# Kernel optimization log

Measured on AMD Instinct MI355X. Metric: run time of the kernel, lower is better.

## Reference

```python
import jax, jax.numpy as jnp
import numpy as np

LOG2PI = 1.8378770664093453
KL_WEIGHT = 1.0
N_OBS = 2_000_000
N_REFL = 250_000
N_IMG = 2000
MC = 32
N_OPS = 2
D_META = 6
D_EMB = 32
D_IN = 2 + 2 + D_META + 2 + D_EMB  # Imodel(2) + Iscale(2) + metadata(6) + wavelength + 1/d^2 + image embed
HIDDEN = 64


def weighted_pearson(x, y, w):
    z = 1.0 / w.sum(-1)
    mx = z * (w * x).sum(-1)
    my = z * (w * y).sum(-1)
    dx = x - mx
    dy = y - my
    cxy = z * (w * dx * dy).sum(-1)
    cx = z * (w * dx * dx).sum(-1)
    cy = z * (w * dy * dy).sum(-1)
    return cxy / jnp.sqrt(cx * cy)


def setup_inputs() -> dict:
    key = jax.random.key(0)
    ks = jax.random.split(key, 16)
    I = jax.random.normal(ks[0], (N_OBS, 1), jnp.float32)
    SigI = jax.random.uniform(ks[1], (N_OBS, 1), jnp.float32, 0.5, 1.5)
    image_id = jnp.sort(jax.random.randint(ks[2], (N_OBS,), 0, N_IMG, jnp.int32))
    metadata = jax.random.normal(ks[3], (N_OBS, D_META), jnp.float32)
    wavelength = 1.0 + 0.1 * jax.random.uniform(ks[4], (N_OBS, 1), jnp.float32)
    dHKL = jax.random.uniform(ks[5], (N_OBS, 1), jnp.float32, 1.0, 4.0)
    refl_ids = jax.random.randint(ks[6], (N_OPS, N_OBS), 0, N_REFL, jnp.int32)
    q_loc = jax.random.normal(ks[7], (N_REFL,), jnp.float32)
    q_scale_raw = 0.1 * jax.random.normal(ks[8], (N_REFL,), jnp.float32)
    img_emb = 0.1 * jax.random.normal(ks[9], (N_IMG, D_EMB), jnp.float32)
    W1 = jax.random.normal(ks[10], (D_IN, HIDDEN), jnp.float32) / np.sqrt(D_IN)
    b1 = jnp.zeros((HIDDEN,), jnp.float32)
    W2 = jax.random.normal(ks[11], (HIDDEN, 2), jnp.float32) / np.sqrt(HIDDEN)
    b2 = jnp.zeros((2,), jnp.float32)
    zeps = jax.random.normal(ks[12], (MC, N_REFL), jnp.float32)
    seps = jax.random.normal(ks[13], (N_OBS, MC), jnp.float32)
    return dict(I=I, SigI=SigI, image_id=image_id, metadata=metadata,
                wavelength=wavelength, dHKL=dHKL, refl_ids=refl_ids,
                q_loc=q_loc, q_scale_raw=q_scale_raw, img_emb=img_emb,
                W1=W1, b1=b1, W2=W2, b2=b2, zeps=zeps, seps=seps)


def reference(I, SigI, image_id, metadata, wavelength, dHKL, refl_ids,
              q_loc, q_scale_raw, img_emb, W1, b1, W2, b2, zeps, seps):
    n_images = img_emb.shape[0]
    sq = jax.nn.softplus(q_scale_raw)                         # q.stddev  [n_refl]
    # KL(N(q_loc, sq) || N(0, 1)), analytic, averaged over reflections
    kl_div = (-jnp.log(sq) + 0.5 * (sq * sq + q_loc * q_loc) - 0.5).mean()
    meta = jnp.concatenate([metadata, wavelength, 1.0 / jnp.square(dHKL)], -1)  # [N, 8]
    Iscale = jnp.concatenate([I, SigI], -1)                   # [N, 2]
    Imodel = jnp.stack([q_loc, sq], -1)                       # [n_refl, 2]
    zT = (q_loc[None, :] + sq[None, :] * zeps).T              # rsample, [n_refl, mc]
    emb = img_emb[image_id]                                   # [N, d_emb]
    ll_list, Ipred_list = [], []
    for op in range(refl_ids.shape[0]):                       # small fixed op count
        rid = refl_ids[op]                                    # [N]
        _Imodel = Imodel[rid]                                 # gather  [N, 2]
        feats = jnp.concatenate([_Imodel, Iscale, meta, emb], -1)
        h = jax.nn.relu(feats @ W1 + b1)
        loc_ls = h @ W2 + b2                                  # [N, 2]
        scale = loc_ls[:, :1] + jax.nn.softplus(loc_ls[:, 1:]) * seps  # [N, mc]
        _Ipred = zT[rid] * scale                              # gather * scale [N, mc]
        _ll = -0.5 * jnp.square((_Ipred - I) / SigI) - jnp.log(SigI) - 0.5 * LOG2PI
        _ll = jax.ops.segment_sum(_ll, image_id, num_segments=n_images)  # [n_img, mc]
        ll_list.append(_ll.mean(-1))                          # [n_img]
        Ipred_list.append(_Ipred.mean(-1))                    # [N]
    ll = jnp.stack(ll_list, -1)                               # [n_img, n_ops]
    ll_max = ll.max(-1)
    op_idx = ll.argmax(-1)                                    # [n_img]
    elbo = -ll_max.mean() + KL_WEIGHT * kl_div
    Ipred = jnp.stack(Ipred_list, -1)                         # [N, n_ops]
    sel = jnp.take_along_axis(Ipred, op_idx[image_id][:, None], -1)[:, 0]
    w = 1.0 / jnp.square(SigI)
    cc = weighted_pearson(I[:, 0], sel, w[:, 0])
    return jnp.stack([elbo, cc])
```

## Files before the change

### kernel.cpp

```cpp
#include <hip/hip_runtime.h>
#include <hip/hip_fp16.h>
#include <math.h>

#define N_OBS_C 2000000
#define N_REFL_C 250000
#define N_IMG_C 2000
#define MC_C 32
#define HID 64
#define NSLOT 16
#define LOG2PI_F 1.8378770664093453f


typedef float f2 __attribute__((ext_vector_type(2)));

__device__ __forceinline__ void pkfma(f2& d, f2 a, f2 b) {
    asm("v_pk_fma_f32 %0, %1, %2, %0" : "+v"(d) : "v"(a), "v"(b));
}
__device__ __forceinline__ f2 pkfma3(f2 a, f2 b, f2 c) {
    f2 d;
    asm("v_pk_fma_f32 %0, %1, %2, %3" : "=v"(d) : "v"(a), "v"(b), "v"(c));
    return d;
}

__device__ __forceinline__ float softplusf(float x) {
    return (x > 20.f) ? x : log1pf(expf(x));
}

#define ZERO_F4 96004
__global__ __launch_bounds__(256) void k_zero(float4* __restrict__ p) {
    int i = blockIdx.x * 256 + threadIdx.x;
    if (i < ZERO_F4) p[i] = make_float4(0.f, 0.f, 0.f, 0.f);
}

__global__ __launch_bounds__(256) void k_refl(const float* __restrict__ q_loc,
                                              const float* __restrict__ q_scale_raw,
                                              const float* __restrict__ zeps,
                                              float* __restrict__ sq,
                                              __half* __restrict__ zT,
                                              double* __restrict__ kl_sum) {
    int r = blockIdx.x * 256 + threadIdx.x;
    double kl = 0.0;
    if (r < N_REFL_C) {
        float ql = q_loc[r];
        float sp = softplusf(q_scale_raw[r]);
        sq[r] = sp;
        kl = (double)(-logf(sp) + 0.5f * (sp * sp + ql * ql) - 0.5f);
        float z[MC_C];
#pragma unroll
        for (int m = 0; m < MC_C; ++m)
            z[m] = fmaf(sp, zeps[(size_t)m * N_REFL_C + r], ql);
        uint4* outp = (uint4*)(zT + (size_t)r * MC_C);
#pragma unroll
        for (int q = 0; q < 4; ++q) {
            __half2 h0 = __floats2half2_rn(z[8 * q + 0], z[8 * q + 1]);
            __half2 h1 = __floats2half2_rn(z[8 * q + 2], z[8 * q + 3]);
            __half2 h2 = __floats2half2_rn(z[8 * q + 4], z[8 * q + 5]);
            __half2 h3 = __floats2half2_rn(z[8 * q + 6], z[8 * q + 7]);
            outp[q] = make_uint4(*(unsigned*)&h0, *(unsigned*)&h1,
                                 *(unsigned*)&h2, *(unsigned*)&h3);
        }
    }
    for (int o = 32; o > 0; o >>= 1) kl += __shfl_xor(kl, o);
    __shared__ double skl[4];
    int lane = threadIdx.x & 63, w = threadIdx.x >> 6;
    if (lane == 0) skl[w] = kl;
    __syncthreads();
    if (threadIdx.x == 0) atomicAdd(kl_sum, skl[0] + skl[1] + skl[2] + skl[3]);
}

__global__ __launch_bounds__(64) void k_imgpre(const float* __restrict__ img_emb,
                                               const float* __restrict__ W1,
                                               const float* __restrict__ b1,
                                               float* __restrict__ img_pre) {
    int g = blockIdx.x;
    int j = threadIdx.x;
    float acc = b1[j];
#pragma unroll
    for (int e = 0; e < 32; ++e)
        acc = fmaf(img_emb[g * 32 + e], W1[(12 + e) * HID + j], acc);
    img_pre[g * HID + j] = acc;
}

__global__ __launch_bounds__(256) void k_mlp(const float* __restrict__ I,
                                             const float* __restrict__ SigI,
                                             const int* __restrict__ image_id,
                                             const float* __restrict__ metadata,
                                             const float* __restrict__ wavelength,
                                             const float* __restrict__ dHKL,
                                             const int* __restrict__ refl_ids,
                                             const float* __restrict__ q_loc,
                                             const float* __restrict__ W1,
                                             const float* __restrict__ W2,
                                             const float* __restrict__ b2,
                                             const float* __restrict__ sq,
                                             const float* __restrict__ img_pre,
                                             float4* __restrict__ params) {
    __shared__ float sW1[12 * HID];
    __shared__ float sW2a[HID], sW2b[HID];
    for (int t = threadIdx.x; t < 12 * HID; t += 256) sW1[t] = W1[t];
    if (threadIdx.x < HID) {
        sW2a[threadIdx.x] = W2[threadIdx.x * 2 + 0];
        sW2b[threadIdx.x] = W2[threadIdx.x * 2 + 1];
    }
    __syncthreads();

    int n0 = blockIdx.x * 512 + threadIdx.x;
    int n1 = n0 + 256;
    bool a0 = (n0 < N_OBS_C), a1 = (n1 < N_OBS_C);
    int m0 = a0 ? n0 : (N_OBS_C - 1);
    int m1 = a1 ? n1 : (N_OBS_C - 1);

    f2 f0p[10], f1p[10];
    {
        float v;
        v = I[m0];            f0p[0].x = v; f0p[0].y = v;
        v = SigI[m0];         f0p[1].x = v; f0p[1].y = v;
#pragma unroll
        for (int i = 0; i < 6; ++i) {
            v = metadata[(size_t)m0 * 6 + i];
            f0p[2 + i].x = v; f0p[2 + i].y = v;
        }
        v = wavelength[m0];   f0p[8].x = v; f0p[8].y = v;
        float dh = dHKL[m0];
        v = 1.0f / (dh * dh); f0p[9].x = v; f0p[9].y = v;

        v = I[m1];            f1p[0].x = v; f1p[0].y = v;
        v = SigI[m1];         f1p[1].x = v; f1p[1].y = v;
#pragma unroll
        for (int i = 0; i < 6; ++i) {
            v = metadata[(size_t)m1 * 6 + i];
            f1p[2 + i].x = v; f1p[2 + i].y = v;
        }
        v = wavelength[m1];   f1p[8].x = v; f1p[8].y = v;
        dh = dHKL[m1];
        v = 1.0f / (dh * dh); f1p[9].x = v; f1p[9].y = v;
    }

    int g0 = image_id[m0], g1 = image_id[m1];
    int r00 = refl_ids[m0], r01 = refl_ids[N_OBS_C + m0];
    int r10 = refl_ids[m1], r11 = refl_ids[N_OBS_C + m1];
    f2 qa0p, sa0p, qb0p, sb0p, qa1p, sa1p, qb1p, sb1p;
    { float v;
      v = q_loc[r00]; qa0p.x = v; qa0p.y = v;
      v = sq[r00];    sa0p.x = v; sa0p.y = v;
      v = q_loc[r01]; qb0p.x = v; qb0p.y = v;
      v = sq[r01];    sb0p.x = v; sb0p.y = v;
      v = q_loc[r10]; qa1p.x = v; qa1p.y = v;
      v = sq[r10];    sa1p.x = v; sa1p.y = v;
      v = q_loc[r11]; qb1p.x = v; qb1p.y = v;
      v = sq[r11];    sb1p.x = v; sb1p.y = v;
    }
    const float* ip0 = img_pre + (size_t)g0 * HID;
    const float* ip1 = img_pre + (size_t)g1 * HID;

    f2 lA00 = {0.f, 0.f}, lA01 = {0.f, 0.f}, lB00 = {0.f, 0.f}, lB01 = {0.f, 0.f};
    f2 lA10 = {0.f, 0.f}, lA11 = {0.f, 0.f}, lB10 = {0.f, 0.f}, lB11 = {0.f, 0.f};

#pragma unroll 1
    for (int jt = 0; jt < HID; jt += 8) {
        f2 ac0[4], ac1[4];
        {
            float4 pa = *(const float4*)&ip0[jt];
            float4 pb = *(const float4*)&ip0[jt + 4];
            ac0[0].x = pa.x; ac0[0].y = pa.y;
            ac0[1].x = pa.z; ac0[1].y = pa.w;
            ac0[2].x = pb.x; ac0[2].y = pb.y;
            ac0[3].x = pb.z; ac0[3].y = pb.w;
            pa = *(const float4*)&ip1[jt];
            pb = *(const float4*)&ip1[jt + 4];
            ac1[0].x = pa.x; ac1[0].y = pa.y;
            ac1[1].x = pa.z; ac1[1].y = pa.w;
            ac1[2].x = pb.x; ac1[2].y = pb.y;
            ac1[3].x = pb.z; ac1[3].y = pb.w;
        }
#pragma unroll
        for (int i = 0; i < 10; ++i) {
            float4 wa = *(const float4*)&sW1[(i + 2) * HID + jt];
            float4 wb = *(const float4*)&sW1[(i + 2) * HID + jt + 4];
            f2 w0; w0.x = wa.x; w0.y = wa.y;
            f2 w1; w1.x = wa.z; w1.y = wa.w;
            f2 w2; w2.x = wb.x; w2.y = wb.y;
            f2 w3; w3.x = wb.z; w3.y = wb.w;
            pkfma(ac0[0], f0p[i], w0); pkfma(ac1[0], f1p[i], w0);
            pkfma(ac0[1], f0p[i], w1); pkfma(ac1[1], f1p[i], w1);
            pkfma(ac0[2], f0p[i], w2); pkfma(ac1[2], f1p[i], w2);
            pkfma(ac0[3], f0p[i], w3); pkfma(ac1[3], f1p[i], w3);
        }
        f2 w0p[4], w1p[4], vap[4], vbp[4];
        {
            float4 wa = *(const float4*)&sW1[jt];
            float4 wb = *(const float4*)&sW1[jt + 4];
            w0p[0].x = wa.x; w0p[0].y = wa.y;
            w0p[1].x = wa.z; w0p[1].y = wa.w;
            w0p[2].x = wb.x; w0p[2].y = wb.y;
            w0p[3].x = wb.z; w0p[3].y = wb.w;
            wa = *(const float4*)&sW1[HID + jt];
            wb = *(const float4*)&sW1[HID + jt + 4];
            w1p[0].x = wa.x; w1p[0].y = wa.y;
            w1p[1].x = wa.z; w1p[1].y = wa.w;
            w1p[2].x = wb.x; w1p[2].y = wb.y;
            w1p[3].x = wb.z; w1p[3].y = wb.w;
            wa = *(const float4*)&sW2a[jt];
            wb = *(const float4*)&sW2a[jt + 4];
            vap[0].x = wa.x; vap[0].y = wa.y;
            vap[1].x = wa.z; vap[1].y = wa.w;
            vap[2].x = wb.x; vap[2].y = wb.y;
            vap[3].x = wb.z; vap[3].y = wb.w;
            wa = *(const float4*)&sW2b[jt];
            wb = *(const float4*)&sW2b[jt + 4];
            vbp[0].x = wa.x; vbp[0].y = wa.y;
            vbp[1].x = wa.z; vbp[1].y = wa.w;
            vbp[2].x = wb.x; vbp[2].y = wb.y;
            vbp[3].x = wb.z; vbp[3].y = wb.w;
        }
#pragma unroll
        for (int k = 0; k < 4; ++k) {
            f2 h;
            h = pkfma3(sa0p, w1p[k], ac0[k]);
            pkfma(h, qa0p, w0p[k]);
            h.x = fmaxf(h.x, 0.f); h.y = fmaxf(h.y, 0.f);
            pkfma(lA00, h, vap[k]);
            pkfma(lA01, h, vbp[k]);
            h = pkfma3(sb0p, w1p[k], ac0[k]);
            pkfma(h, qb0p, w0p[k]);
            h.x = fmaxf(h.x, 0.f); h.y = fmaxf(h.y, 0.f);
            pkfma(lB00, h, vap[k]);
            pkfma(lB01, h, vbp[k]);
            h = pkfma3(sa1p, w1p[k], ac1[k]);
            pkfma(h, qa1p, w0p[k]);
            h.x = fmaxf(h.x, 0.f); h.y = fmaxf(h.y, 0.f);
            pkfma(lA10, h, vap[k]);
            pkfma(lA11, h, vbp[k]);
            h = pkfma3(sb1p, w1p[k], ac1[k]);
            pkfma(h, qb1p, w0p[k]);
            h.x = fmaxf(h.x, 0.f); h.y = fmaxf(h.y, 0.f);
            pkfma(lB10, h, vap[k]);
            pkfma(lB11, h, vbp[k]);
        }
    }

    float bb0 = b2[0], bb1 = b2[1];
    if (a0) {
        float la0 = bb0 + lA00.x + lA00.y;
        float la1 = bb1 + lA01.x + lA01.y;
        float lb0 = bb0 + lB00.x + lB00.y;
        float lb1 = bb1 + lB01.x + lB01.y;
        params[n0] = make_float4(la0, softplusf(la1), lb0, softplusf(lb1));
    }
    if (a1) {
        float la0 = bb0 + lA10.x + lA10.y;
        float la1 = bb1 + lA11.x + lA11.y;
        float lb0 = bb0 + lB10.x + lB10.y;
        float lb1 = bb1 + lB11.x + lB11.y;
        params[n1] = make_float4(la0, softplusf(la1), lb0, softplusf(lb1));
    }
}

__global__ __launch_bounds__(256) void k_mc(const float* __restrict__ I,
                                            const float* __restrict__ SigI,
                                            const int* __restrict__ image_id,
                                            const int* __restrict__ refl_ids,
                                            const float4* __restrict__ params,
                                            const float* __restrict__ seps,
                                            const __half* __restrict__ zT,
                                            float* __restrict__ img_mom) {
    int t = threadIdx.x;
    int grp = t >> 3;
    int m4 = t & 7;
    int n = blockIdx.x * 32 + grp;

    float In = I[n];
    float Sn = SigI[n];
    int g = image_id[n];
    int rid0 = refl_ids[n];
    int rid1 = refl_ids[N_OBS_C + n];
    float4 pp = params[n];

    float4 ss = *(const float4*)&seps[(size_t)n * MC_C + m4 * 4];
    float4 z0, z1;
    {
        const __half2* zp = (const __half2*)(zT + (size_t)rid0 * MC_C + m4 * 4);
        __half2 h0 = zp[0], h1 = zp[1];
        float2 fa = __half22float2(h0), fb = __half22float2(h1);
        z0 = make_float4(fa.x, fa.y, fb.x, fb.y);
        zp = (const __half2*)(zT + (size_t)rid1 * MC_C + m4 * 4);
        h0 = zp[0]; h1 = zp[1];
        fa = __half22float2(h0); fb = __half22float2(h1);
        z1 = make_float4(fa.x, fa.y, fb.x, fb.y);
    }

    float rsig = 1.0f / Sn;
    float mnIr = -In * rsig;

    float sd20 = 0.f, sip0 = 0.f, sd21 = 0.f, sip1 = 0.f;
#define MCSTEP(zc0, zc1, sc_)                              \
    {                                                      \
        float sc0 = fmaf(pp.y, sc_, pp.x);                 \
        float ip0 = zc0 * sc0;                             \
        float d0 = fmaf(ip0, rsig, mnIr);                  \
        sd20 = fmaf(d0, d0, sd20);                         \
        sip0 += ip0;                                       \
        float sc1 = fmaf(pp.w, sc_, pp.z);                 \
        float ip1 = zc1 * sc1;                             \
        float d1 = fmaf(ip1, rsig, mnIr);                  \
        sd21 = fmaf(d1, d1, sd21);                         \
        sip1 += ip1;                                       \
    }
    MCSTEP(z0.x, z1.x, ss.x)
    MCSTEP(z0.y, z1.y, ss.y)
    MCSTEP(z0.z, z1.z, ss.z)
    MCSTEP(z0.w, z1.w, ss.w)
#undef MCSTEP

#pragma unroll
    for (int o = 4; o > 0; o >>= 1) {
        sd20 += __shfl_xor(sd20, o);
        sd21 += __shfl_xor(sd21, o);
        sip0 += __shfl_xor(sip0, o);
        sip1 += __shfl_xor(sip1, o);
    }

    __shared__ float mom[32][12];
    __shared__ int sg[32];
    __shared__ int sameflag;
    if (m4 == 0) {
        float logS32 = 32.f * logf(Sn) + 16.f * LOG2PI_F;
        float y0 = sip0 * (1.0f / 32.0f);
        float y1 = sip1 * (1.0f / 32.0f);
        float w = rsig * rsig;
        mom[grp][0] = -0.5f * sd20 - logS32;
        mom[grp][1] = -0.5f * sd21 - logS32;
        mom[grp][2] = w;
        mom[grp][3] = w * In;
        mom[grp][4] = w * In * In;
        mom[grp][5] = w * y0;
        mom[grp][6] = w * y0 * y0;
        mom[grp][7] = w * In * y0;
        mom[grp][8] = w * y1;
        mom[grp][9] = w * y1 * y1;
        mom[grp][10] = w * In * y1;
        mom[grp][11] = 0.f;
        sg[grp] = g;
    }
    __syncthreads();
    if (t == 0) {
        bool same = true;
        int g0 = sg[0];
#pragma unroll
        for (int s = 1; s < 32; ++s) same = same && (sg[s] == g0);
        sameflag = same;
    }
    __syncthreads();
    int slot = blockIdx.x & (NSLOT - 1);
    if (t < 12) {
        if (sameflag) {
            float a = 0.f;
#pragma unroll
            for (int s = 0; s < 32; ++s) a += mom[s][t];
            atomicAdd(&img_mom[(sg[0] * 12 + t) * NSLOT + slot], a);
        } else {
            for (int s = 0; s < 32; ++s)
                atomicAdd(&img_mom[(sg[s] * 12 + t) * NSLOT + slot], mom[s][t]);
        }
    }
}

__global__ __launch_bounds__(256) void k_img(const float* __restrict__ img_mom,
                                             double* __restrict__ accs) {
    int g = blockIdx.x * 256 + threadIdx.x;
    double red7[7] = {0, 0, 0, 0, 0, 0, 0};
    if (g < N_IMG_C) {
        float M[12];
#pragma unroll
        for (int j = 0; j < 12; ++j) {
            const float4* p = (const float4*)&img_mom[(g * 12 + j) * NSLOT];
            float4 q0 = p[0], q1 = p[1], q2 = p[2], q3 = p[3];
            M[j] = (q0.x + q0.y + q0.z + q0.w) + (q1.x + q1.y + q1.z + q1.w) +
                   (q2.x + q2.y + q2.z + q2.w) + (q3.x + q3.y + q3.z + q3.w);
        }
        float ll0 = M[0] * (1.0f / 32.0f);
        float ll1 = M[1] * (1.0f / 32.0f);
        bool op1 = (ll1 > ll0);
        red7[0] = (double)fmaxf(ll0, ll1);
        red7[1] = (double)M[2];
        red7[2] = (double)M[3];
        red7[3] = (double)(op1 ? M[8] : M[5]);
        red7[4] = (double)M[4];
        red7[5] = (double)(op1 ? M[9] : M[6]);
        red7[6] = (double)(op1 ? M[10] : M[7]);
    }
#pragma unroll
    for (int k = 0; k < 7; ++k)
        for (int o = 32; o > 0; o >>= 1) red7[k] += __shfl_xor(red7[k], o);
    __shared__ double sred[4][7];
    int lane = threadIdx.x & 63, w = threadIdx.x >> 6;
    if (lane == 0) {
#pragma unroll
        for (int k = 0; k < 7; ++k) sred[w][k] = red7[k];
    }
    __syncthreads();
    if (threadIdx.x < 7) {
        double v = sred[0][threadIdx.x] + sred[1][threadIdx.x] +
                   sred[2][threadIdx.x] + sred[3][threadIdx.x];
        atomicAdd(&accs[1 + threadIdx.x], v);
    }
}

__global__ void k_final(const double* __restrict__ accs, float* __restrict__ out) {
    double kl = accs[0] / (double)N_REFL_C;
    double elbo = -(accs[1] / (double)N_IMG_C) + 1.0 * kl;
    double W = accs[2], Sx = accs[3], Sy = accs[4];
    double Sxx = accs[5], Syy = accs[6], Sxy = accs[7];
    double z = 1.0 / W;
    double mx = z * Sx, my = z * Sy;
    double cxy = z * Sxy - mx * my;
    double cx = z * Sxx - mx * mx;
    double cy = z * Syy - my * my;
    double cc = cxy / sqrt(cx * cy);
    out[0] = (float)elbo;
    out[1] = (float)cc;
}

extern "C" void kernel_launch(void* const* d_in, const int* in_sizes, int n_in,
                              void* d_out, int out_size, void* d_ws, size_t ws_size,
                              hipStream_t stream) {
    const float* I = (const float*)d_in[0];
    const float* SigI = (const float*)d_in[1];
    const int* image_id = (const int*)d_in[2];
    const float* metadata = (const float*)d_in[3];
    const float* wavelength = (const float*)d_in[4];
    const float* dHKL = (const float*)d_in[5];
    const int* refl_ids = (const int*)d_in[6];
    const float* q_loc = (const float*)d_in[7];
    const float* q_scale_raw = (const float*)d_in[8];
    const float* img_emb = (const float*)d_in[9];
    const float* W1 = (const float*)d_in[10];
    const float* b1 = (const float*)d_in[11];
    const float* W2 = (const float*)d_in[12];
    const float* b2 = (const float*)d_in[13];
    const float* zeps = (const float*)d_in[14];
    const float* seps = (const float*)d_in[15];
    float* out = (float*)d_out;

    char* ws = (char*)d_ws;
    double* accs = (double*)ws;
    float* img_mom = (float*)(ws + 64);
    float* sqv = (float*)(ws + 2097152);
    float* img_pre = (float*)(ws + 4194304);
    __half* zT = (__half*)(ws + 8388608);
    float4* params = (float4*)(ws + 50331648);

    k_zero<<<(ZERO_F4 + 255) / 256, 256, 0, stream>>>((float4*)ws);
    k_refl<<<(N_REFL_C + 255) / 256, 256, 0, stream>>>(q_loc, q_scale_raw, zeps,
                                                       sqv, zT, &accs[0]);
    k_imgpre<<<N_IMG_C, 64, 0, stream>>>(img_emb, W1, b1, img_pre);
    k_mlp<<<(N_OBS_C + 511) / 512, 256, 0, stream>>>(I, SigI, image_id, metadata,
                                                     wavelength, dHKL, refl_ids,
                                                     q_loc, W1, W2, b2, sqv,
                                                     img_pre, params);
    k_mc<<<N_OBS_C / 32, 256, 0, stream>>>(I, SigI, image_id, refl_ids,
                                           params, seps, zT, img_mom);
    k_img<<<(N_IMG_C + 255) / 256, 256, 0, stream>>>(img_mom, accs);
    k_final<<<1, 1, 0, stream>>>(accs, out);
}
```

Before: 262.8 us.

## Fuse MLP and Monte-Carlo likelihood kernels into one block-local pass

Merges the per-observation MLP kernel and the MC sampling/reduction kernel into a single kernel. MLP outputs, I/SigI, reflection ids and image ids are kept in shared memory, so the params buffer no longer goes to global memory and per-observation inputs are not reloaded. The MC stage then walks 16 chunks of 32 observations per block, and the per-image moment atomics are batched in two halves. The cost is more shared memory and more barriers per block, which lowers occupancy, and the MC phase now runs at coarser per-block granularity.

```diff
diff --git a/kernel.cpp b/kernel.cpp
--- a/kernel.cpp
+++ b/kernel.cpp
@@ -81,40 +81,51 @@
     img_pre[g * HID + j] = acc;
 }
 
-__global__ __launch_bounds__(256) void k_mlp(const float* __restrict__ I,
-                                             const float* __restrict__ SigI,
-                                             const int* __restrict__ image_id,
-                                             const float* __restrict__ metadata,
-                                             const float* __restrict__ wavelength,
-                                             const float* __restrict__ dHKL,
-                                             const int* __restrict__ refl_ids,
-                                             const float* __restrict__ q_loc,
-                                             const float* __restrict__ W1,
-                                             const float* __restrict__ W2,
-                                             const float* __restrict__ b2,
-                                             const float* __restrict__ sq,
-                                             const float* __restrict__ img_pre,
-                                             float4* __restrict__ params) {
+__global__ __launch_bounds__(256) void k_main(const float* __restrict__ I,
+                                              const float* __restrict__ SigI,
+                                              const int* __restrict__ image_id,
+                                              const float* __restrict__ metadata,
+                                              const float* __restrict__ wavelength,
+                                              const float* __restrict__ dHKL,
+                                              const int* __restrict__ refl_ids,
+                                              const float* __restrict__ q_loc,
+                                              const float* __restrict__ W1,
+                                              const float* __restrict__ W2,
+                                              const float* __restrict__ b2,
+                                              const float* __restrict__ sq,
+                                              const float* __restrict__ img_pre,
+                                              const float* __restrict__ seps,
+                                              const __half* __restrict__ zT,
+                                              float* __restrict__ img_mom) {
     __shared__ float sW1[12 * HID];
     __shared__ float sW2a[HID], sW2b[HID];
-    for (int t = threadIdx.x; t < 12 * HID; t += 256) sW1[t] = W1[t];
-    if (threadIdx.x < HID) {
-        sW2a[threadIdx.x] = W2[threadIdx.x * 2 + 0];
-        sW2b[threadIdx.x] = W2[threadIdx.x * 2 + 1];
-    }
-    __syncthreads();
-
-    int n0 = blockIdx.x * 512 + threadIdx.x;
+    __shared__ float4 pms[512];
+    __shared__ float2 sIS[512];
+    __shared__ int2 srid[512];
+    __shared__ int sgid[512];
+    __shared__ float mom[8][32][12];
+    __shared__ int sflag[16];
+
+    int tid = threadIdx.x;
+    for (int t = tid; t < 12 * HID; t += 256) sW1[t] = W1[t];
+    if (tid < HID) {
+        sW2a[tid] = W2[tid * 2 + 0];
+        sW2b[tid] = W2[tid * 2 + 1];
+    }
+
+    int n0 = blockIdx.x * 512 + tid;
     int n1 = n0 + 256;
     bool a0 = (n0 < N_OBS_C), a1 = (n1 < N_OBS_C);
     int m0 = a0 ? n0 : (N_OBS_C - 1);
     int m1 = a1 ? n1 : (N_OBS_C - 1);
 
+    float I0 = I[m0], I1 = I[m1];
+    float S0 = SigI[m0], S1 = SigI[m1];
     f2 f0p[10], f1p[10];
     {
         float v;
-        v = I[m0];            f0p[0].x = v; f0p[0].y = v;
-        v = SigI[m0];         f0p[1].x = v; f0p[1].y = v;
+        f0p[0].x = I0; f0p[0].y = I0;
+        f0p[1].x = S0; f0p[1].y = S0;
 #pragma unroll
         for (int i = 0; i < 6; ++i) {
             v = metadata[(size_t)m0 * 6 + i];
@@ -124,8 +135,8 @@
         float dh = dHKL[m0];
         v = 1.0f / (dh * dh); f0p[9].x = v; f0p[9].y = v;
 
-        v = I[m1];            f1p[0].x = v; f1p[0].y = v;
-        v = SigI[m1];         f1p[1].x = v; f1p[1].y = v;
+        f1p[0].x = I1; f1p[0].y = I1;
+        f1p[1].x = S1; f1p[1].y = S1;
 #pragma unroll
         for (int i = 0; i < 6; ++i) {
             v = metadata[(size_t)m1 * 6 + i];
@@ -135,7 +146,6 @@
         dh = dHKL[m1];
         v = 1.0f / (dh * dh); f1p[9].x = v; f1p[9].y = v;
     }
-
     int g0 = image_id[m0], g1 = image_id[m1];
     int r00 = refl_ids[m0], r01 = refl_ids[N_OBS_C + m0];
     int r10 = refl_ids[m1], r11 = refl_ids[N_OBS_C + m1];
@@ -152,6 +162,15 @@
     }
     const float* ip0 = img_pre + (size_t)g0 * HID;
     const float* ip1 = img_pre + (size_t)g1 * HID;
+
+    sIS[tid] = make_float2(I0, S0);
+    sIS[tid + 256] = make_float2(I1, S1);
+    srid[tid] = make_int2(r00, r01);
+    srid[tid + 256] = make_int2(r10, r11);
+    sgid[tid] = a0 ? g0 : -1;
+    sgid[tid + 256] = a1 ? g1 : -1;
+
+    __syncthreads();
 
     f2 lA00 = {0.f, 0.f}, lA01 = {0.f, 0.f}, lB00 = {0.f, 0.f}, lB01 = {0.f, 0.f};
     f2 lA10 = {0.f, 0.f}, lA11 = {0.f, 0.f}, lB10 = {0.f, 0.f}, lB11 = {0.f, 0.f};
@@ -239,129 +258,119 @@
         }
     }
 
-    float bb0 = b2[0], bb1 = b2[1];
-    if (a0) {
-        float la0 = bb0 + lA00.x + lA00.y;
-        float la1 = bb1 + lA01.x + lA01.y;
-        float lb0 = bb0 + lB00.x + lB00.y;
-        float lb1 = bb1 + lB01.x + lB01.y;
-        params[n0] = make_float4(la0, softplusf(la1), lb0, softplusf(lb1));
-    }
-    if (a1) {
-        float la0 = bb0 + lA10.x + lA10.y;
-        float la1 = bb1 + lA11.x + lA11.y;
-        float lb0 = bb0 + lB10.x + lB10.y;
-        float lb1 = bb1 + lB11.x + lB11.y;
-        params[n1] = make_float4(la0, softplusf(la1), lb0, softplusf(lb1));
-    }
-}
-
-__global__ __launch_bounds__(256) void k_mc(const float* __restrict__ I,
-                                            const float* __restrict__ SigI,
-                                            const int* __restrict__ image_id,
-                                            const int* __restrict__ refl_ids,
-                                            const float4* __restrict__ params,
-                                            const float* __restrict__ seps,
-                                            const __half* __restrict__ zT,
-                                            float* __restrict__ img_mom) {
-    int t = threadIdx.x;
-    int grp = t >> 3;
-    int m4 = t & 7;
-    int n = blockIdx.x * 32 + grp;
-
-    float In = I[n];
-    float Sn = SigI[n];
-    int g = image_id[n];
-    int rid0 = refl_ids[n];
-    int rid1 = refl_ids[N_OBS_C + n];
-    float4 pp = params[n];
-
-    float4 ss = *(const float4*)&seps[(size_t)n * MC_C + m4 * 4];
-    float4 z0, z1;
     {
-        const __half2* zp = (const __half2*)(zT + (size_t)rid0 * MC_C + m4 * 4);
-        __half2 h0 = zp[0], h1 = zp[1];
-        float2 fa = __half22float2(h0), fb = __half22float2(h1);
-        z0 = make_float4(fa.x, fa.y, fb.x, fb.y);
-        zp = (const __half2*)(zT + (size_t)rid1 * MC_C + m4 * 4);
-        h0 = zp[0]; h1 = zp[1];
-        fa = __half22float2(h0); fb = __half22float2(h1);
-        z1 = make_float4(fa.x, fa.y, fb.x, fb.y);
-    }
-
-    float rsig = 1.0f / Sn;
-    float mnIr = -In * rsig;
-
-    float sd20 = 0.f, sip0 = 0.f, sd21 = 0.f, sip1 = 0.f;
+        float bb0 = b2[0], bb1 = b2[1];
+        pms[tid] = make_float4(bb0 + lA00.x + lA00.y, softplusf(bb1 + lA01.x + lA01.y),
+                               bb0 + lB00.x + lB00.y, softplusf(bb1 + lB01.x + lB01.y));
+        pms[tid + 256] = make_float4(bb0 + lA10.x + lA10.y, softplusf(bb1 + lA11.x + lA11.y),
+                                     bb0 + lB10.x + lB10.y, softplusf(bb1 + lB11.x + lB11.y));
+    }
+    __syncthreads();
+
+    if (tid < 16) sflag[tid] = (sgid[tid * 32] == sgid[tid * 32 + 31]) ? 1 : 0;
+    __syncthreads();
+
+    int grp = tid >> 3;
+    int m4 = tid & 7;
+
+    for (int half = 0; half < 2; ++half) {
+#pragma unroll 2
+        for (int cc = 0; cc < 8; ++cc) {
+            int c = half * 8 + cc;
+            int o = c * 32 + grp;
+            int nn = blockIdx.x * 512 + o;
+            if (nn >= N_OBS_C) nn = N_OBS_C - 1;
+            int2 rr = srid[o];
+            float4 pp = pms[o];
+            float2 IS = sIS[o];
+
+            float4 ss = *(const float4*)&seps[(size_t)nn * MC_C + m4 * 4];
+            float4 z0, z1;
+            {
+                const __half2* zp = (const __half2*)(zT + (size_t)rr.x * MC_C + m4 * 4);
+                __half2 h0 = zp[0], h1 = zp[1];
+                float2 fa = __half22float2(h0), fb = __half22float2(h1);
+                z0 = make_float4(fa.x, fa.y, fb.x, fb.y);
+                zp = (const __half2*)(zT + (size_t)rr.y * MC_C + m4 * 4);
+                h0 = zp[0]; h1 = zp[1];
+                fa = __half22float2(h0); fb = __half22float2(h1);
+                z1 = make_float4(fa.x, fa.y, fb.x, fb.y);
+            }
+
+            float rsig = 1.0f / IS.y;
+            float mnIr = -IS.x * rsig;
+
+            float sd20 = 0.f, sip0 = 0.f, sd21 = 0.f, sip1 = 0.f;
 #define MCSTEP(zc0, zc1, sc_)                              \
-    {                                                      \
-        float sc0 = fmaf(pp.y, sc_, pp.x);                 \
-        float ip0 = zc0 * sc0;                             \
-        float d0 = fmaf(ip0, rsig, mnIr);                  \
-        sd20 = fmaf(d0, d0, sd20);                         \
-        sip0 += ip0;                                       \
-        float sc1 = fmaf(pp.w, sc_, pp.z);                 \
-        float ip1 = zc1 * sc1;                             \
-        float d1 = fmaf(ip1, rsig, mnIr);                  \
-        sd21 = fmaf(d1, d1, sd21);                         \
-        sip1 += ip1;                                       \
-    }
-    MCSTEP(z0.x, z1.x, ss.x)
-    MCSTEP(z0.y, z1.y, ss.y)
-    MCSTEP(z0.z, z1.z, ss.z)
-    MCSTEP(z0.w, z1.w, ss.w)
+            {                                              \
+                float sc0 = fmaf(pp.y, sc_, pp.x);         \
+                float ip0 = zc0 * sc0;                     \
+                float d0 = fmaf(ip0, rsig, mnIr);          \
+                sd20 = fmaf(d0, d0, sd20);                 \
+                sip0 += ip0;                               \
+                float sc1 = fmaf(pp.w, sc_, pp.z);         \
+                float ip1 = zc1 * sc1;                     \
+                float d1 = fmaf(ip1, rsig, mnIr);          \
+                sd21 = fmaf(d1, d1, sd21);                 \
+                sip1 += ip1;                               \
+            }
+            MCSTEP(z0.x, z1.x, ss.x)
+            MCSTEP(z0.y, z1.y, ss.y)
+            MCSTEP(z0.z, z1.z, ss.z)
+            MCSTEP(z0.w, z1.w, ss.w)
 #undef MCSTEP
 
 #pragma unroll
-    for (int o = 4; o > 0; o >>= 1) {
-        sd20 += __shfl_xor(sd20, o);
-        sd21 += __shfl_xor(sd21, o);
-        sip0 += __shfl_xor(sip0, o);
-        sip1 += __shfl_xor(sip1, o);
-    }
-
-    __shared__ float mom[32][12];
-    __shared__ int sg[32];
-    __shared__ int sameflag;
-    if (m4 == 0) {
-        float logS32 = 32.f * logf(Sn) + 16.f * LOG2PI_F;
-        float y0 = sip0 * (1.0f / 32.0f);
-        float y1 = sip1 * (1.0f / 32.0f);
-        float w = rsig * rsig;
-        mom[grp][0] = -0.5f * sd20 - logS32;
-        mom[grp][1] = -0.5f * sd21 - logS32;
-        mom[grp][2] = w;
-        mom[grp][3] = w * In;
-        mom[grp][4] = w * In * In;
-        mom[grp][5] = w * y0;
-        mom[grp][6] = w * y0 * y0;
-        mom[grp][7] = w * In * y0;
-        mom[grp][8] = w * y1;
-        mom[grp][9] = w * y1 * y1;
-        mom[grp][10] = w * In * y1;
-        mom[grp][11] = 0.f;
-        sg[grp] = g;
-    }
-    __syncthreads();
-    if (t == 0) {
-        bool same = true;
-        int g0 = sg[0];
-#pragma unroll
-        for (int s = 1; s < 32; ++s) same = same && (sg[s] == g0);
-        sameflag = same;
-    }
-    __syncthreads();
-    int slot = blockIdx.x & (NSLOT - 1);
-    if (t < 12) {
-        if (sameflag) {
-            float a = 0.f;
-#pragma unroll
-            for (int s = 0; s < 32; ++s) a += mom[s][t];
-            atomicAdd(&img_mom[(sg[0] * 12 + t) * NSLOT + slot], a);
-        } else {
-            for (int s = 0; s < 32; ++s)
-                atomicAdd(&img_mom[(sg[s] * 12 + t) * NSLOT + slot], mom[s][t]);
-        }
+            for (int o2 = 4; o2 > 0; o2 >>= 1) {
+                sd20 += __shfl_xor(sd20, o2);
+                sd21 += __shfl_xor(sd21, o2);
+                sip0 += __shfl_xor(sip0, o2);
+                sip1 += __shfl_xor(sip1, o2);
+            }
+
+            if (m4 == 0) {
+                float logS32 = 32.f * logf(IS.y) + 16.f * LOG2PI_F;
+                float y0 = sip0 * (1.0f / 32.0f);
+                float y1 = sip1 * (1.0f / 32.0f);
+                float w = rsig * rsig;
+                float* mr = mom[cc][grp];
+                mr[0] = -0.5f * sd20 - logS32;
+                mr[1] = -0.5f * sd21 - logS32;
+                mr[2] = w;
+                mr[3] = w * IS.x;
+                mr[4] = w * IS.x * IS.x;
+                mr[5] = w * y0;
+                mr[6] = w * y0 * y0;
+                mr[7] = w * IS.x * y0;
+                mr[8] = w * y1;
+                mr[9] = w * y1 * y1;
+                mr[10] = w * IS.x * y1;
+                mr[11] = 0.f;
+            }
+        }
+        __syncthreads();
+
+        if (tid < 96) {
+            int cc = tid / 12, j = tid - cc * 12;
+            int c = half * 8 + cc;
+            int slot = blockIdx.x & (NSLOT - 1);
+            if (sflag[c]) {
+                int gg = sgid[c * 32];
+                if (gg >= 0) {
+                    float v = 0.f;
+#pragma unroll
+                    for (int s = 0; s < 32; ++s) v += mom[cc][s][j];
+                    atomicAdd(&img_mom[(gg * 12 + j) * NSLOT + slot], v);
+                }
+            } else {
+                for (int s = 0; s < 32; ++s) {
+                    int gs = sgid[c * 32 + s];
+                    if (gs >= 0)
+                        atomicAdd(&img_mom[(gs * 12 + j) * NSLOT + slot], mom[cc][s][j]);
+                }
+            }
+        }
+        __syncthreads();
     }
 }
 
@@ -448,18 +457,15 @@
     float* sqv = (float*)(ws + 2097152);
     float* img_pre = (float*)(ws + 4194304);
     __half* zT = (__half*)(ws + 8388608);
-    float4* params = (float4*)(ws + 50331648);
 
     k_zero<<<(ZERO_F4 + 255) / 256, 256, 0, stream>>>((float4*)ws);
     k_refl<<<(N_REFL_C + 255) / 256, 256, 0, stream>>>(q_loc, q_scale_raw, zeps,
                                                        sqv, zT, &accs[0]);
     k_imgpre<<<N_IMG_C, 64, 0, stream>>>(img_emb, W1, b1, img_pre);
-    k_mlp<<<(N_OBS_C + 511) / 512, 256, 0, stream>>>(I, SigI, image_id, metadata,
-                                                     wavelength, dHKL, refl_ids,
-                                                     q_loc, W1, W2, b2, sqv,
-                                                     img_pre, params);
-    k_mc<<<N_OBS_C / 32, 256, 0, stream>>>(I, SigI, image_id, refl_ids,
-                                           params, seps, zT, img_mom);
+    k_main<<<(N_OBS_C + 511) / 512, 256, 0, stream>>>(I, SigI, image_id, metadata,
+                                                      wavelength, dHKL, refl_ids,
+                                                      q_loc, W1, W2, b2, sqv,
+                                                      img_pre, seps, zT, img_mom);
     k_img<<<(N_IMG_C + 255) / 256, 256, 0, stream>>>(img_mom, accs);
     k_final<<<1, 1, 0, stream>>>(accs, out);
 }
```

Result: slower. 274.1 us (+4.3%).
